# Optimization experiments

Hardware: AMD Instinct MI355X
Metric: run time of the kernel (lower is better)

Reference implementation:

```python
import jax, jax.numpy as jnp
import numpy as np

NUM_HEADS = 12
HEAD_DIM = 64


def setup_inputs() -> dict:
    key = jax.random.key(0)
    ks = jax.random.split(key, 8)
    B, S, D, M = 8, 1024, 768, 8
    scale = 0.02
    return {
        "hidden_states": jax.random.normal(ks[0], (B, S, D), jnp.float32),
        "memory": jax.random.normal(ks[1], (1, M, D), jnp.float32) * scale,
        "Wq": jax.random.normal(ks[2], (D, D), jnp.float32) * scale,
        "bq": jnp.zeros((D,), jnp.float32),
        "Wk": jax.random.normal(ks[3], (D, D), jnp.float32) * scale,
        "bk": jnp.zeros((D,), jnp.float32),
        "Wv": jax.random.normal(ks[4], (D, D), jnp.float32) * scale,
        "bv": jnp.zeros((D,), jnp.float32),
    }


def _split_heads(x):
    # (B, S, D) -> (B, H, S, Dh)
    B, S, _ = x.shape
    return x.reshape(B, S, NUM_HEADS, HEAD_DIM).transpose(0, 2, 1, 3)


def reference(hidden_states, memory, Wq, bq, Wk, bk, Wv, bv):
    B, S, D = hidden_states.shape
    # prepend? no: memory tokens are concatenated AFTER hidden_states on token dim
    mem = jnp.broadcast_to(memory, (B,) + memory.shape[1:])
    with_memory = jnp.concatenate([hidden_states, mem], axis=1)  # (B, S+M, D)

    # torch nn.Linear: x @ W.T + b
    q = _split_heads(hidden_states @ Wq.T + bq)   # (B, H, S,   Dh)
    k = _split_heads(with_memory @ Wk.T + bk)     # (B, H, S+M, Dh)
    v = _split_heads(with_memory @ Wv.T + bv)     # (B, H, S+M, Dh)

    scaling = 1.0 / np.sqrt(HEAD_DIM).astype(np.float32)
    scores = jnp.einsum("bhqd,bhkd->bhqk", q, k) * scaling
    probs = jax.nn.softmax(scores, axis=-1)  # dropout is identity in eval
    ctx = jnp.einsum("bhqk,bhkd->bhqd", probs, v)  # (B, H, S, Dh)
    ctx = ctx.transpose(0, 2, 1, 3).reshape(B, S, D)
    return ctx
```

## Files before the change

### kernel.cpp

```cpp
#include <hip/hip_runtime.h>

typedef unsigned short ushort_t;
typedef __attribute__((ext_vector_type(8))) short bf16x8;
typedef __attribute__((ext_vector_type(4))) short s16x4;
typedef __attribute__((ext_vector_type(4))) float f32x4;

#define BATCH 8
#define SEQ   1024
#define MEMT  8
#define LREAL 1032
#define LPAD  1152
#define DMODEL 768
#define NH    12
#define DH    64

#define CEXP 0.18033688011112042f

__device__ __forceinline__ ushort_t f2b(float x) {
  union { float f; unsigned u; } c; c.f = x;
  unsigned u = c.u;
  unsigned r = (u + 0x7fffu + ((u >> 16) & 1u)) >> 16;
  return (ushort_t)r;
}

#if defined(__has_builtin)
#if __has_builtin(__builtin_amdgcn_global_load_lds)
#define HAVE_GLL 1
#endif
#if __has_builtin(__builtin_amdgcn_exp2f)
#define EXP2F(x) __builtin_amdgcn_exp2f(x)
#endif
#endif
#ifndef EXP2F
#define EXP2F(x) __expf((x) * 0.6931471805599453f)
#endif

__device__ __forceinline__ void stage16(const ushort_t* g, ushort_t* lds_wave_base) {
#ifdef HAVE_GLL
  __builtin_amdgcn_global_load_lds(
      (const __attribute__((address_space(1))) unsigned int*)g,
      (__attribute__((address_space(3))) unsigned int*)lds_wave_base,
      16, 0, 0);
#else
  int lane = threadIdx.x & 63;
  *(bf16x8*)(lds_wave_base + lane * 8) = *(const bf16x8*)g;
#endif
}

__global__ __launch_bounds__(256) void prep(const float* __restrict__ hidden,
                                            const float* __restrict__ memv,
                                            const float* __restrict__ Wq,
                                            const float* __restrict__ Wk,
                                            const float* __restrict__ Wv,
                                            ushort_t* __restrict__ Xm,
                                            ushort_t* __restrict__ Wqb,
                                            ushort_t* __restrict__ Wkb,
                                            ushort_t* __restrict__ Wvb) {
  int bx = blockIdx.x;
  if (bx < 6912) {
    size_t idx = ((size_t)bx * 256 + threadIdx.x) * 4;
    const size_t perB = (size_t)LPAD * DMODEL;
    int b = (int)(idx / perB);
    size_t rem = idx - (size_t)b * perB;
    int row = (int)(rem / DMODEL);
    int col = (int)(rem - (size_t)row * DMODEL);
    f32x4 v;
    if (row < SEQ) {
      v = *(const f32x4*)(hidden + ((size_t)b * SEQ + row) * DMODEL + col);
    } else if (row < LREAL) {
      v = *(const f32x4*)(memv + (size_t)(row - SEQ) * DMODEL + col);
    } else {
      v = (f32x4){0.f, 0.f, 0.f, 0.f};
    }
    s16x4 p;
    p[0] = (short)f2b(v[0]); p[1] = (short)f2b(v[1]);
    p[2] = (short)f2b(v[2]); p[3] = (short)f2b(v[3]);
    *(s16x4*)(Xm + idx) = p;
  } else {
    int t = bx - 6912;
    int m = t / 576;
    int i = (t - m * 576) * 256 + threadIdx.x;
    const float* src = m == 0 ? Wq : (m == 1 ? Wk : Wv);
    ushort_t* dst = m == 0 ? Wqb : (m == 1 ? Wkb : Wvb);
    f32x4 v = *(const f32x4*)(src + (size_t)i * 4);
    s16x4 p;
    p[0] = (short)f2b(v[0]); p[1] = (short)f2b(v[1]);
    p[2] = (short)f2b(v[2]); p[3] = (short)f2b(v[3]);
    *(s16x4*)(dst + (size_t)i * 4) = p;
  }
}

__global__ __launch_bounds__(512, 4) void gemm_fused(
    const ushort_t* __restrict__ Xm,
    const ushort_t* __restrict__ Wqb, const ushort_t* __restrict__ Wkb,
    const ushort_t* __restrict__ Wvb,
    const float* __restrict__ bq, const float* __restrict__ bk,
    const float* __restrict__ bv,
    ushort_t* __restrict__ Qb, ushort_t* __restrict__ Kb,
    ushort_t* __restrict__ Vtb) {
  __shared__ __align__(16) ushort_t S[17408];
  ushort_t* As = S;
  ushort_t* Bs = S + 8192;

  const int tid = threadIdx.x;
  const int wave = tid >> 6, lane = tid & 63;
  const int quad = lane >> 4, l15 = lane & 15;
  const int wm = wave >> 2, wn = wave & 3;

  int bx = blockIdx.x;
  int task, xt, yt, b;
  if (bx < 432) {
    int slot = bx & 7, rest = bx >> 3;
    int y = rest % 6, vhi = rest / 6;
    int v = slot + 8 * vhi;
    task = 2; xt = v % 9; b = v / 9; yt = y;
  } else if (bx < 816) {
    int t = bx - 432;
    int slot = t & 7, rest = t >> 3;
    int x = rest % 6, qhi = rest / 6;
    int q = slot + 8 * qhi;
    task = 0; xt = x; yt = q & 7; b = q >> 3;
  } else {
    int t = bx - 816;
    int slot = t & 7, rest = t >> 3;
    int x = rest % 6, khi = rest / 6;
    int k = slot + 8 * khi;
    task = 1; xt = x; yt = k % 9; b = k / 9;
  }
  const int rowTile = yt * 128, colTile = xt * 128;
  const ushort_t* Xb = Xm + (size_t)b * LPAD * DMODEL;
  const ushort_t* A = task == 2 ? Wvb : Xb;
  const ushort_t* W = task == 2 ? Xb : (task == 0 ? Wqb : Wkb);
  const float* bias = task == 2 ? bv : (task == 0 ? bq : bk);

  const int lrow4 = lane >> 2, lcol8 = (lane & 3) << 3;

  f32x4 acc[4][2] = {};

  for (int k0 = 0; k0 < DMODEL; k0 += 64) {
#pragma unroll
    for (int s = 0; s < 4; ++s) {
      int u = wave * 4 + s;
      int x = u & 15;
      int kk = x >> 3, rg = x & 7;
      int lb = kk * 4096 + rg * 512;
      if (u < 16) {
        stage16(A + (size_t)(rowTile + rg * 16 + lrow4) * DMODEL + k0 + kk * 32 + lcol8,
                As + lb);
      } else {
        stage16(W + (size_t)(colTile + rg * 16 + lrow4) * DMODEL + k0 + kk * 32 + lcol8,
                Bs + lb);
      }
    }
    __syncthreads();
#pragma unroll
    for (int kk = 0; kk < 2; ++kk) {
      bf16x8 af[4], bfr[2];
#pragma unroll
      for (int mt = 0; mt < 4; ++mt)
        af[mt] = *(const bf16x8*)&As[kk * 4096 + (wm * 64 + mt * 16 + l15) * 32 + quad * 8];
#pragma unroll
      for (int nt = 0; nt < 2; ++nt)
        bfr[nt] = *(const bf16x8*)&Bs[kk * 4096 + (wn * 32 + nt * 16 + l15) * 32 + quad * 8];
#pragma unroll
      for (int mt = 0; mt < 4; ++mt)
#pragma unroll
        for (int nt = 0; nt < 2; ++nt)
          acc[mt][nt] = __builtin_amdgcn_mfma_f32_16x16x32_bf16(af[mt], bfr[nt], acc[mt][nt], 0, 0, 0);
    }
    __syncthreads();
  }

  const float scale = task == 0 ? CEXP : 1.0f;
#pragma unroll
  for (int mt = 0; mt < 4; ++mt)
#pragma unroll
    for (int nt = 0; nt < 2; ++nt) {
      int lr0 = wm * 64 + mt * 16 + quad * 4;
      int lc = wn * 32 + nt * 16 + l15;
#pragma unroll
      for (int r = 0; r < 4; ++r) {
        float bsv = (task == 2) ? bias[rowTile + lr0 + r] : bias[colTile + lc];
        S[(lr0 + r) * 136 + lc] = f2b((acc[mt][nt][r] + bsv) * scale);
      }
    }
  __syncthreads();

  {
    int row = tid >> 2;
    int segu = (tid & 3) * 32;
    bf16x8 v0 = *(const bf16x8*)&S[row * 136 + segu + 0];
    bf16x8 v1 = *(const bf16x8*)&S[row * 136 + segu + 8];
    bf16x8 v2 = *(const bf16x8*)&S[row * 136 + segu + 16];
    bf16x8 v3 = *(const bf16x8*)&S[row * 136 + segu + 24];
    if (task == 2) {
      int d = rowTile + row;
      ushort_t* gp = Vtb + (((size_t)b * NH + (d >> 6)) * DH + (d & 63)) * LPAD + colTile + segu;
      *(bf16x8*)(gp + 0) = v0;  *(bf16x8*)(gp + 8) = v1;
      *(bf16x8*)(gp + 16) = v2; *(bf16x8*)(gp + 24) = v3;
    } else {
      ushort_t* out = task == 0 ? Qb : Kb;
      const int Rows = task == 0 ? SEQ : LPAD;
      int colbase = colTile + segu;
      int h = colbase >> 6, dd = colbase & 63;
      ushort_t* gp = out + (((size_t)b * NH + h) * Rows + rowTile + row) * DH + dd;
      *(bf16x8*)(gp + 0) = v0;  *(bf16x8*)(gp + 8) = v1;
      *(bf16x8*)(gp + 16) = v2; *(bf16x8*)(gp + 24) = v3;
    }
  }
}

__global__ __launch_bounds__(256, 3) void attn(const ushort_t* __restrict__ Q,
                                               const ushort_t* __restrict__ K,
                                               const ushort_t* __restrict__ Vt,
                                               float* __restrict__ Out) {
  __shared__ __align__(16) ushort_t Ks[2 * 4096];
  __shared__ __align__(16) ushort_t Vs[4 * 2048];
  __shared__ __align__(16) ushort_t Ps[4 * 2304];

  const int tid = threadIdx.x, wave = tid >> 6, lane = tid & 63;
  const int quad = lane >> 4, l15 = lane & 15;
  const int bh = blockIdx.x, qt = blockIdx.y;
  const int h = bh % NH, b = bh / NH;

  const ushort_t* Qp = Q + (((size_t)b * NH + h) * SEQ + qt * 128) * DH;
  const ushort_t* Kp = K + ((size_t)b * NH + h) * LPAD * DH;
  const ushort_t* Vp = Vt + ((size_t)b * NH + h) * DH * LPAD;
  ushort_t* Pw = Ps + wave * 2304;

  bf16x8 qf[2][2];
#pragma unroll
  for (int mt = 0; mt < 2; ++mt)
#pragma unroll
    for (int kk = 0; kk < 2; ++kk)
      qf[mt][kk] = *(const bf16x8*)&Qp[(wave * 32 + mt * 16 + l15) * DH + kk * 32 + quad * 8];

  bf16x8 ones8;
#pragma unroll
  for (int j = 0; j < 8; ++j) ones8[j] = (short)0x3f80;

  f32x4 ob[2][4] = {};
  f32x4 obl[2] = {};

  const int srow = tid >> 2;
  const int scol = (tid & 3) << 3;

  for (int kt = 0; kt < 9; ++kt) {
    const int key0 = kt * 128;
#pragma unroll
    for (int kk = 0; kk < 2; ++kk)
#pragma unroll
      for (int is = 0; is < 2; ++is) {
        int krow = is * 64 + srow;
        stage16(Kp + (size_t)(key0 + krow) * DH + kk * 32 + scol,
                Ks + kk * 4096 + is * 2048 + wave * 512);
      }
#pragma unroll
    for (int kc = 0; kc < 4; ++kc)
      stage16(Vp + (size_t)srow * LPAD + key0 + kc * 32 + scol,
              Vs + kc * 2048 + wave * 512);
    __syncthreads();

#pragma unroll
    for (int half = 0; half < 2; ++half) {
      f32x4 sc[2][4] = {};
#pragma unroll
      for (int kk = 0; kk < 2; ++kk)
#pragma unroll
        for (int nt = 0; nt < 4; ++nt) {
          bf16x8 kf = *(const bf16x8*)&Ks[kk * 4096 + (half * 64 + nt * 16 + l15) * 32 + quad * 8];
#pragma unroll
          for (int mt = 0; mt < 2; ++mt)
            sc[mt][nt] = __builtin_amdgcn_mfma_f32_16x16x32_bf16(qf[mt][kk], kf, sc[mt][nt], 0, 0, 0);
        }

      if (kt < 8) {
#pragma unroll
        for (int mt = 0; mt < 2; ++mt)
#pragma unroll
          for (int nt = 0; nt < 4; ++nt)
#pragma unroll
            for (int r = 0; r < 4; ++r) {
              union { float f; unsigned u; } cu;
              cu.f = EXP2F(sc[mt][nt][r]);
              Pw[(mt * 16 + quad * 4 + r) * 72 + nt * 16 + l15] = (ushort_t)(cu.u >> 16);
            }
      } else {
#pragma unroll
        for (int mt = 0; mt < 2; ++mt)
#pragma unroll
          for (int nt = 0; nt < 4; ++nt) {
            int key = key0 + half * 64 + nt * 16 + l15;
            bool valid = key < LREAL;
#pragma unroll
            for (int r = 0; r < 4; ++r) {
              union { float f; unsigned u; } cu;
              cu.f = valid ? EXP2F(sc[mt][nt][r]) : 0.f;
              Pw[(mt * 16 + quad * 4 + r) * 72 + nt * 16 + l15] = (ushort_t)(cu.u >> 16);
            }
          }
      }

#pragma unroll
      for (int kc2 = 0; kc2 < 2; ++kc2) {
        int kcg = half * 2 + kc2;
        bf16x8 pf[2];
#pragma unroll
        for (int mt = 0; mt < 2; ++mt)
          pf[mt] = *(const bf16x8*)&Pw[(mt * 16 + l15) * 72 + kc2 * 32 + quad * 8];
#pragma unroll
        for (int dt = 0; dt < 4; ++dt) {
          bf16x8 vf = *(const bf16x8*)&Vs[kcg * 2048 + (dt * 16 + l15) * 32 + quad * 8];
#pragma unroll
          for (int mt = 0; mt < 2; ++mt)
            ob[mt][dt] = __builtin_amdgcn_mfma_f32_16x16x32_bf16(pf[mt], vf, ob[mt][dt], 0, 0, 0);
        }
#pragma unroll
        for (int mt = 0; mt < 2; ++mt)
          obl[mt] = __builtin_amdgcn_mfma_f32_16x16x32_bf16(pf[mt], ones8, obl[mt], 0, 0, 0);
      }
    }
    __syncthreads();
  }

#pragma unroll
  for (int mt = 0; mt < 2; ++mt) {
    int row0 = qt * 128 + wave * 32 + mt * 16 + quad * 4;
    f32x4 linv;
#pragma unroll
    for (int r = 0; r < 4; ++r) linv[r] = 1.0f / obl[mt][r];
#pragma unroll
    for (int dt = 0; dt < 4; ++dt) {
      int col = h * DH + dt * 16 + l15;
#pragma unroll
      for (int r = 0; r < 4; ++r)
        Out[((size_t)b * SEQ + row0 + r) * DMODEL + col] = ob[mt][dt][r] * linv[r];
    }
  }
}

extern "C" void kernel_launch(void* const* d_in, const int* in_sizes, int n_in,
                              void* d_out, int out_size, void* d_ws, size_t ws_size,
                              hipStream_t stream) {
  const float* hidden = (const float*)d_in[0];
  const float* memv   = (const float*)d_in[1];
  const float* Wq = (const float*)d_in[2];
  const float* bq = (const float*)d_in[3];
  const float* Wk = (const float*)d_in[4];
  const float* bk = (const float*)d_in[5];
  const float* Wv = (const float*)d_in[6];
  const float* bv = (const float*)d_in[7];
  float* out = (float*)d_out;

  char* ws = (char*)d_ws;
  size_t off = 0;
  ushort_t* Xm  = (ushort_t*)(ws + off); off += (size_t)BATCH * LPAD * DMODEL * 2;
  ushort_t* Wqb = (ushort_t*)(ws + off); off += (size_t)DMODEL * DMODEL * 2;
  ushort_t* Wkb = (ushort_t*)(ws + off); off += (size_t)DMODEL * DMODEL * 2;
  ushort_t* Wvb = (ushort_t*)(ws + off); off += (size_t)DMODEL * DMODEL * 2;
  ushort_t* Qb  = (ushort_t*)(ws + off); off += (size_t)BATCH * NH * SEQ * DH * 2;
  ushort_t* Kb  = (ushort_t*)(ws + off); off += (size_t)BATCH * NH * LPAD * DH * 2;
  ushort_t* Vtb = (ushort_t*)(ws + off);

  prep<<<dim3(8640), 256, 0, stream>>>(hidden, memv, Wq, Wk, Wv, Xm, Wqb, Wkb, Wvb);
  gemm_fused<<<dim3(1248), 512, 0, stream>>>(Xm, Wqb, Wkb, Wvb, bq, bk, bv, Qb, Kb, Vtb);
  attn<<<dim3(96, 8), 256, 0, stream>>>(Qb, Kb, Vtb, out);
}
```

Baseline: 185.6 us.

## Double-buffer LDS staging in projection GEMM and attention key loop

Result: faster. 181.7 us (-2.1%).

```diff
diff --git a/kernel.cpp b/kernel.cpp
--- a/kernel.cpp
+++ b/kernel.cpp
@@ -58,12 +58,12 @@
                                             ushort_t* __restrict__ Wvb) {
   int bx = blockIdx.x;
   if (bx < 6912) {
-    size_t idx = ((size_t)bx * 256 + threadIdx.x) * 4;
-    const size_t perB = (size_t)LPAD * DMODEL;
-    int b = (int)(idx / perB);
-    size_t rem = idx - (size_t)b * perB;
-    int row = (int)(rem / DMODEL);
-    int col = (int)(rem - (size_t)row * DMODEL);
+    unsigned idx = ((unsigned)bx * 256u + threadIdx.x) * 4u;
+    const unsigned perB = (unsigned)LPAD * DMODEL;
+    unsigned b = idx / perB;
+    unsigned rem = idx - b * perB;
+    unsigned row = rem / DMODEL;
+    unsigned col = rem - row * DMODEL;
     f32x4 v;
     if (row < SEQ) {
       v = *(const f32x4*)(hidden + ((size_t)b * SEQ + row) * DMODEL + col);
@@ -99,13 +99,12 @@
     ushort_t* __restrict__ Qb, ushort_t* __restrict__ Kb,
     ushort_t* __restrict__ Vtb) {
   __shared__ __align__(16) ushort_t S[17408];
-  ushort_t* As = S;
-  ushort_t* Bs = S + 8192;
 
   const int tid = threadIdx.x;
   const int wave = tid >> 6, lane = tid & 63;
   const int quad = lane >> 4, l15 = lane & 15;
   const int wm = wave >> 2, wn = wave & 3;
+  const int lrow4 = lane >> 2, lcol8 = (lane & 3) << 3;
 
   int bx = blockIdx.x;
   int task, xt, yt, b;
@@ -133,41 +132,35 @@
   const ushort_t* W = task == 2 ? Xb : (task == 0 ? Wqb : Wkb);
   const float* bias = task == 2 ? bv : (task == 0 ? bq : bk);
 
-  const int lrow4 = lane >> 2, lcol8 = (lane & 3) << 3;
+  const ushort_t* Arow = A + (size_t)(rowTile + wave * 16 + lrow4) * DMODEL + lcol8;
+  const ushort_t* Wrow = W + (size_t)(colTile + wave * 16 + lrow4) * DMODEL + lcol8;
 
   f32x4 acc[4][2] = {};
 
-  for (int k0 = 0; k0 < DMODEL; k0 += 64) {
-#pragma unroll
-    for (int s = 0; s < 4; ++s) {
-      int u = wave * 4 + s;
-      int x = u & 15;
-      int kk = x >> 3, rg = x & 7;
-      int lb = kk * 4096 + rg * 512;
-      if (u < 16) {
-        stage16(A + (size_t)(rowTile + rg * 16 + lrow4) * DMODEL + k0 + kk * 32 + lcol8,
-                As + lb);
-      } else {
-        stage16(W + (size_t)(colTile + rg * 16 + lrow4) * DMODEL + k0 + kk * 32 + lcol8,
-                Bs + lb);
-      }
-    }
-    __syncthreads();
-#pragma unroll
-    for (int kk = 0; kk < 2; ++kk) {
-      bf16x8 af[4], bfr[2];
-#pragma unroll
-      for (int mt = 0; mt < 4; ++mt)
-        af[mt] = *(const bf16x8*)&As[kk * 4096 + (wm * 64 + mt * 16 + l15) * 32 + quad * 8];
+  stage16(Arow, S + wave * 512);
+  stage16(Wrow, S + 4096 + wave * 512);
+  __syncthreads();
+
+  for (int i = 0; i < 24; ++i) {
+    ushort_t* cur = S + ((i & 1) << 13);
+    if (i < 23) {
+      ushort_t* nxt = S + (((i + 1) & 1) << 13);
+      int k0n = (i + 1) * 32;
+      stage16(Arow + k0n, nxt + wave * 512);
+      stage16(Wrow + k0n, nxt + 4096 + wave * 512);
+    }
+    bf16x8 af[4], bfr[2];
+#pragma unroll
+    for (int mt = 0; mt < 4; ++mt)
+      af[mt] = *(const bf16x8*)&cur[(wm * 64 + mt * 16 + l15) * 32 + quad * 8];
+#pragma unroll
+    for (int nt = 0; nt < 2; ++nt)
+      bfr[nt] = *(const bf16x8*)&cur[4096 + (wn * 32 + nt * 16 + l15) * 32 + quad * 8];
+#pragma unroll
+    for (int mt = 0; mt < 4; ++mt)
 #pragma unroll
       for (int nt = 0; nt < 2; ++nt)
-        bfr[nt] = *(const bf16x8*)&Bs[kk * 4096 + (wn * 32 + nt * 16 + l15) * 32 + quad * 8];
-#pragma unroll
-      for (int mt = 0; mt < 4; ++mt)
-#pragma unroll
-        for (int nt = 0; nt < 2; ++nt)
-          acc[mt][nt] = __builtin_amdgcn_mfma_f32_16x16x32_bf16(af[mt], bfr[nt], acc[mt][nt], 0, 0, 0);
-    }
+        acc[mt][nt] = __builtin_amdgcn_mfma_f32_16x16x32_bf16(af[mt], bfr[nt], acc[mt][nt], 0, 0, 0);
     __syncthreads();
   }
 
@@ -214,12 +207,12 @@
                                                const ushort_t* __restrict__ K,
                                                const ushort_t* __restrict__ Vt,
                                                float* __restrict__ Out) {
-  __shared__ __align__(16) ushort_t Ks[2 * 4096];
-  __shared__ __align__(16) ushort_t Vs[4 * 2048];
+  __shared__ __align__(16) ushort_t KV[16384];
   __shared__ __align__(16) ushort_t Ps[4 * 2304];
 
   const int tid = threadIdx.x, wave = tid >> 6, lane = tid & 63;
   const int quad = lane >> 4, l15 = lane & 15;
+  const int lrow4 = lane >> 2, lcol8 = (lane & 3) << 3;
   const int bh = blockIdx.x, qt = blockIdx.y;
   const int h = bh % NH, b = bh / NH;
 
@@ -242,83 +235,83 @@
   f32x4 ob[2][4] = {};
   f32x4 obl[2] = {};
 
-  const int srow = tid >> 2;
-  const int scol = (tid & 3) << 3;
-
-  for (int kt = 0; kt < 9; ++kt) {
-    const int key0 = kt * 128;
+#define STAGE_KV(key0_, buf_)                                                        \
+  {                                                                                  \
+    _Pragma("unroll")                                                                \
+    for (int s = 0; s < 2; ++s) {                                                    \
+      int c = wave + s * 4;                                                          \
+      int hi = c >> 2, lo = c & 3;                                                   \
+      stage16(Kp + (size_t)((key0_) + lo * 16 + lrow4) * DH + hi * 32 + lcol8,       \
+              (buf_) + c * 512);                                                     \
+      stage16(Vp + (size_t)(lo * 16 + lrow4) * LPAD + (key0_) + hi * 32 + lcol8,     \
+              (buf_) + 4096 + c * 512);                                              \
+    }                                                                                \
+  }
+
+  STAGE_KV(0, KV)
+  __syncthreads();
+
+  for (int kt = 0; kt < 17; ++kt) {
+    ushort_t* cur = KV + ((kt & 1) << 13);
+    if (kt < 16) {
+      ushort_t* nxt = KV + (((kt + 1) & 1) << 13);
+      STAGE_KV((kt + 1) * 64, nxt)
+    }
+
+    f32x4 sc[2][4] = {};
 #pragma unroll
     for (int kk = 0; kk < 2; ++kk)
 #pragma unroll
-      for (int is = 0; is < 2; ++is) {
-        int krow = is * 64 + srow;
-        stage16(Kp + (size_t)(key0 + krow) * DH + kk * 32 + scol,
-                Ks + kk * 4096 + is * 2048 + wave * 512);
+      for (int nt = 0; nt < 4; ++nt) {
+        bf16x8 kf = *(const bf16x8*)&cur[kk * 2048 + (nt * 16 + l15) * 32 + quad * 8];
+#pragma unroll
+        for (int mt = 0; mt < 2; ++mt)
+          sc[mt][nt] = __builtin_amdgcn_mfma_f32_16x16x32_bf16(qf[mt][kk], kf, sc[mt][nt], 0, 0, 0);
       }
-#pragma unroll
-    for (int kc = 0; kc < 4; ++kc)
-      stage16(Vp + (size_t)srow * LPAD + key0 + kc * 32 + scol,
-              Vs + kc * 2048 + wave * 512);
-    __syncthreads();
-
-#pragma unroll
-    for (int half = 0; half < 2; ++half) {
-      f32x4 sc[2][4] = {};
-#pragma unroll
-      for (int kk = 0; kk < 2; ++kk)
+
+    if (kt < 16) {
+#pragma unroll
+      for (int mt = 0; mt < 2; ++mt)
+#pragma unroll
+        for (int nt = 0; nt < 4; ++nt)
+#pragma unroll
+          for (int r = 0; r < 4; ++r) {
+            union { float f; unsigned u; } cu;
+            cu.f = EXP2F(sc[mt][nt][r]);
+            Pw[(mt * 16 + quad * 4 + r) * 72 + nt * 16 + l15] = (ushort_t)(cu.u >> 16);
+          }
+    } else {
+      bool valid0 = (l15 < 8);
+#pragma unroll
+      for (int mt = 0; mt < 2; ++mt)
 #pragma unroll
         for (int nt = 0; nt < 4; ++nt) {
-          bf16x8 kf = *(const bf16x8*)&Ks[kk * 4096 + (half * 64 + nt * 16 + l15) * 32 + quad * 8];
-#pragma unroll
-          for (int mt = 0; mt < 2; ++mt)
-            sc[mt][nt] = __builtin_amdgcn_mfma_f32_16x16x32_bf16(qf[mt][kk], kf, sc[mt][nt], 0, 0, 0);
+          bool valid = (nt == 0) && valid0;
+#pragma unroll
+          for (int r = 0; r < 4; ++r) {
+            union { float f; unsigned u; } cu;
+            cu.f = valid ? EXP2F(sc[mt][nt][r]) : 0.f;
+            Pw[(mt * 16 + quad * 4 + r) * 72 + nt * 16 + l15] = (ushort_t)(cu.u >> 16);
+          }
         }
-
-      if (kt < 8) {
+    }
+
+#pragma unroll
+    for (int kc = 0; kc < 2; ++kc) {
+      bf16x8 pf[2];
+#pragma unroll
+      for (int mt = 0; mt < 2; ++mt)
+        pf[mt] = *(const bf16x8*)&Pw[(mt * 16 + l15) * 72 + kc * 32 + quad * 8];
+#pragma unroll
+      for (int dt = 0; dt < 4; ++dt) {
+        bf16x8 vf = *(const bf16x8*)&cur[4096 + kc * 2048 + (dt * 16 + l15) * 32 + quad * 8];
 #pragma unroll
         for (int mt = 0; mt < 2; ++mt)
-#pragma unroll
-          for (int nt = 0; nt < 4; ++nt)
-#pragma unroll
-            for (int r = 0; r < 4; ++r) {
-              union { float f; unsigned u; } cu;
-              cu.f = EXP2F(sc[mt][nt][r]);
-              Pw[(mt * 16 + quad * 4 + r) * 72 + nt * 16 + l15] = (ushort_t)(cu.u >> 16);
-            }
-      } else {
-#pragma unroll
-        for (int mt = 0; mt < 2; ++mt)
-#pragma unroll
-          for (int nt = 0; nt < 4; ++nt) {
-            int key = key0 + half * 64 + nt * 16 + l15;
-            bool valid = key < LREAL;
-#pragma unroll
-            for (int r = 0; r < 4; ++r) {
-              union { float f; unsigned u; } cu;
-              cu.f = valid ? EXP2F(sc[mt][nt][r]) : 0.f;
-              Pw[(mt * 16 + quad * 4 + r) * 72 + nt * 16 + l15] = (ushort_t)(cu.u >> 16);
-            }
-          }
+          ob[mt][dt] = __builtin_amdgcn_mfma_f32_16x16x32_bf16(pf[mt], vf, ob[mt][dt], 0, 0, 0);
       }
-
-#pragma unroll
-      for (int kc2 = 0; kc2 < 2; ++kc2) {
-        int kcg = half * 2 + kc2;
-        bf16x8 pf[2];
-#pragma unroll
-        for (int mt = 0; mt < 2; ++mt)
-          pf[mt] = *(const bf16x8*)&Pw[(mt * 16 + l15) * 72 + kc2 * 32 + quad * 8];
-#pragma unroll
-        for (int dt = 0; dt < 4; ++dt) {
-          bf16x8 vf = *(const bf16x8*)&Vs[kcg * 2048 + (dt * 16 + l15) * 32 + quad * 8];
-#pragma unroll
-          for (int mt = 0; mt < 2; ++mt)
-            ob[mt][dt] = __builtin_amdgcn_mfma_f32_16x16x32_bf16(pf[mt], vf, ob[mt][dt], 0, 0, 0);
-        }
-#pragma unroll
-        for (int mt = 0; mt < 2; ++mt)
-          obl[mt] = __builtin_amdgcn_mfma_f32_16x16x32_bf16(pf[mt], ones8, obl[mt], 0, 0, 0);
-      }
+#pragma unroll
+      for (int mt = 0; mt < 2; ++mt)
+        obl[mt] = __builtin_amdgcn_mfma_f32_16x16x32_bf16(pf[mt], ones8, obl[mt], 0, 0, 0);
     }
     __syncthreads();
   }
```
